# Optimization experiments

Measured on AMD Instinct MI355X. Metric: run time of the kernel, lower is better.

Reference implementation:

```python
import jax, jax.numpy as jnp
import numpy as np

B, S, T, H, E, V = 64, 512, 12, 256, 256, 50000


def _xavier(key, shape):
    lim = np.sqrt(6.0 / (shape[0] + shape[1]))
    return jax.random.uniform(key, shape, jnp.float32, -lim, lim)


def setup_inputs() -> dict:
    key = jax.random.key(0)
    ks = jax.random.split(key, 14)
    return {
        "input_ids": jax.random.randint(ks[0], (B, S), 0, V),
        "tree_ids": jax.random.randint(ks[1], (B, T, S), 0, S),
        "tree_ids_r": jax.random.randint(ks[2], (B, T, S), 0, S),
        "tree_ids_l": jax.random.randint(ks[3], (B, T, S), 0, S),
        "emb": _xavier(ks[4], (V, E)),
        "W_ioux": _xavier(ks[5], (E, 3 * H)),
        "b_ioux": jnp.zeros((3 * H,), jnp.float32),
        "U_iou_r": _xavier(ks[6], (H, 3 * H)),
        "U_iou_l": _xavier(ks[7], (H, 3 * H)),
        "W_f": _xavier(ks[8], (E, H)),
        "b_f": jnp.zeros((H,), jnp.float32),
        "U_f0": _xavier(ks[9], (H, H)),
        "U_f1": _xavier(ks[10], (H, H)),
        "U_f2": _xavier(ks[11], (H, H)),
        "U_f3": _xavier(ks[12], (H, H)),
    }


def reference(input_ids, tree_ids, tree_ids_r, tree_ids_l, emb,
              W_ioux, b_ioux, U_iou_r, U_iou_l, W_f, b_f,
              U_f0, U_f1, U_f2, U_f3):
    x = emb[input_ids]                      # [B, S, E]
    Bn, Sn = x.shape[0], x.shape[1]
    Hn = U_f0.shape[0]
    bidx = jnp.arange(Bn)[:, None]          # [B, 1] batch index for scatter

    def take(a, idx):                       # gather along node dim: out[b,s]=a[b,idx[b,s]]
        return jnp.take_along_axis(a, idx[..., None], axis=1)

    iou_x = x @ W_ioux + b_ioux             # precompute; constant across steps
    f_x = x @ W_f + b_f

    def step(carry, ids):
        h, c = carry
        td, tr, tl = ids                    # each [B, S]
        # which parent nodes receive children this step (node 0 excluded)
        counts = jnp.zeros((Bn, Sn), x.dtype).at[bidx, td].add(1.0)
        mask = (counts.at[:, 0].set(0.0) > 0)[..., None]  # [B, S, 1]
        # scatter-add child hidden projections into parent iou preactivations
        iou = iou_x.at[bidx, tr].add(h @ U_iou_r)
        iou = iou.at[bidx, tl].add(h @ U_iou_l)
        i, o, u = jnp.split(iou, 3, axis=-1)
        i, o, u = jax.nn.sigmoid(i), jax.nn.sigmoid(o), jnp.tanh(u)
        # forget gate per child: gather parent fx and child-hidden projections
        f = jax.nn.sigmoid(take(f_x, td)
                           + take(h @ U_f0 + h @ U_f1, tr)
                           + take(h @ U_f2 + h @ U_f3, tl))
        c_new = (i * u).at[bidx, td].add(f * c)
        h_new = o * jnp.tanh(c_new)
        h = jnp.where(mask, h_new, h)
        c = jnp.where(mask, c_new, c)
        return (h, c), None

    h0 = jnp.zeros((Bn, Sn, Hn), x.dtype)
    ids = (jnp.swapaxes(tree_ids, 0, 1),
           jnp.swapaxes(tree_ids_r, 0, 1),
           jnp.swapaxes(tree_ids_l, 0, 1))   # [T, B, S]
    (h, c), _ = jax.lax.scan(step, (h0, h0), ids)

    roots = tree_ids[:, -1, :].max(axis=1)   # [B]
    h_root = h[jnp.arange(Bn), roots]        # [B, H]
    return h, c, h_root
```

## Files before the change

### kernel.cpp

```cpp
#include <hip/hip_runtime.h>
#include <stdint.h>

#define B_ 64
#define S_ 512
#define T_ 12
#define M_ (B_*S_)
#define NP_ 2048

typedef __attribute__((ext_vector_type(8))) short bf16x8;
typedef __attribute__((ext_vector_type(4))) float f32x4;

__device__ __forceinline__ uint16_t f2bf(float f){
  union { float f; uint32_t u; } x; x.f = f;
  uint32_t r = x.u + 0x7FFFu + ((x.u >> 16) & 1u);
  return (uint16_t)(r >> 16);
}
__device__ __forceinline__ float bf2f(uint16_t u){
  union { float f; uint32_t u; } x; x.u = ((uint32_t)u) << 16; return x.f;
}
__device__ __forceinline__ float sigm(float x){ return 1.0f/(1.0f + expf(-x)); }
__device__ __forceinline__ float4 bf4(const uint16_t* p){
  const ushort4 v = *reinterpret_cast<const ushort4*>(p);
  return make_float4(bf2f(v.x), bf2f(v.y), bf2f(v.z), bf2f(v.w));
}

__device__ __forceinline__ void gload16(const uint16_t* g, uint16_t* l){
  __builtin_amdgcn_global_load_lds(
      (const __attribute__((address_space(1))) uint32_t*)g,
      (__attribute__((address_space(3))) uint32_t*)l, 16, 0, 0);
}

__global__ void zero16(uint4* __restrict__ p, long n16){
  const long i = (long)blockIdx.x * 256 + threadIdx.x;
  if (i < n16) p[i] = make_uint4(0,0,0,0);
}
__global__ void bf16_to_f32(const uint16_t* __restrict__ src, float* __restrict__ dst, long n){
  const long i = ((long)blockIdx.x * 256 + threadIdx.x) * 4;
  if (i + 3 < n) {
    const float4 o = bf4(src + i);
    *reinterpret_cast<float4*>(dst + i) = o;
  }
}

__global__ void build_ucatT(const float* __restrict__ Ur, const float* __restrict__ Ul,
                            const float* __restrict__ f0, const float* __restrict__ f1,
                            const float* __restrict__ f2, const float* __restrict__ f3,
                            uint16_t* __restrict__ UcatT){
  const int idx = blockIdx.x * 256 + threadIdx.x;
  const int n = idx >> 8, k = idx & 255;
  float v;
  if (n < 768)        v = Ur[k*768 + n];
  else if (n < 1536)  v = Ul[k*768 + (n-768)];
  else if (n < 1792) { int j = n-1536; v = f0[k*256+j] + f1[k*256+j]; }
  else               { int j = n-1792; v = f2[k*256+j] + f3[k*256+j]; }
  UcatT[(long)n*256 + k] = f2bf(v);
}

__global__ void build_wallT(const float* __restrict__ Wioux, const float* __restrict__ Wf,
                            uint16_t* __restrict__ WT){
  const int idx = blockIdx.x * 256 + threadIdx.x;
  const int n = idx >> 8, k = idx & 255;
  const float v = (n < 768) ? Wioux[(long)k*768 + n] : Wf[(long)k*256 + (n-768)];
  WT[(long)n*256 + k] = f2bf(v);
}

__global__ __launch_bounds__(256)
void mfma_gemm(const float* __restrict__ Af, const int* __restrict__ row_ids,
               const uint16_t* __restrict__ BT,
               const float* __restrict__ bias, const float* __restrict__ bias2, int split,
               uint16_t* __restrict__ C, int N)
{
  __shared__ uint16_t As[128][40];
  __shared__ uint16_t Bs[128][40];
  const int tid  = threadIdx.x;
  const int lane = tid & 63;
  const int wave = tid >> 6;
  const int wr = wave >> 1, wc = wave & 1;
  const long m0 = (long)blockIdx.y * 128;
  const int  n0 = blockIdx.x * 128;

  const int srow = tid >> 1;
  const int sseg = (tid & 1) * 16;
  const long arid = (long)row_ids[m0 + srow];

  f32x4 acc[4][4];
  #pragma unroll
  for (int i=0;i<4;i++)
    #pragma unroll
    for (int j=0;j<4;j++) acc[i][j] = (f32x4){0.f,0.f,0.f,0.f};

  for (int ks = 0; ks < 256; ks += 32) {
    {
      const float* sf = Af + arid*256 + ks + sseg;
      uint16_t tmp[16];
      #pragma unroll
      for (int e=0;e<16;e++) tmp[e] = f2bf(sf[e]);
      *reinterpret_cast<uint4*>(&As[srow][sseg])     = *reinterpret_cast<const uint4*>(&tmp[0]);
      *reinterpret_cast<uint4*>(&As[srow][sseg + 8]) = *reinterpret_cast<const uint4*>(&tmp[8]);
    }
    {
      const uint16_t* src = BT + (long)(n0 + srow)*256 + ks + sseg;
      *reinterpret_cast<uint4*>(&Bs[srow][sseg])     = *reinterpret_cast<const uint4*>(src);
      *reinterpret_cast<uint4*>(&Bs[srow][sseg + 8]) = *reinterpret_cast<const uint4*>(src + 8);
    }
    __syncthreads();

    bf16x8 af[4], bfv[4];
    #pragma unroll
    for (int i=0;i<4;i++)
      af[i] = *reinterpret_cast<const bf16x8*>(&As[wr*64 + i*16 + (lane & 15)][(lane >> 4)*8]);
    #pragma unroll
    for (int j=0;j<4;j++)
      bfv[j] = *reinterpret_cast<const bf16x8*>(&Bs[wc*64 + j*16 + (lane & 15)][(lane >> 4)*8]);
    #pragma unroll
    for (int i=0;i<4;i++)
      #pragma unroll
      for (int j=0;j<4;j++)
        acc[i][j] = __builtin_amdgcn_mfma_f32_16x16x32_bf16(af[i], bfv[j], acc[i][j], 0, 0, 0);
    __syncthreads();
  }

  const int col16 = lane & 15, rquad = lane >> 4;
  #pragma unroll
  for (int j=0;j<4;j++){
    const int col = n0 + wc*64 + j*16 + col16;
    const float bv = (col < split) ? bias[col] : bias2[col - split];
    #pragma unroll
    for (int i=0;i<4;i++){
      const long rbase = m0 + wr*64 + i*16 + rquad*4;
      #pragma unroll
      for (int r=0;r<4;r++)
        C[(rbase + r)*N + col] = f2bf(acc[i][j][r] + bv);
    }
  }
}

__global__ __launch_bounds__(256)
void gemm_step(const uint16_t* __restrict__ A, const uint16_t* __restrict__ BT,
               uint16_t* __restrict__ C, int N)
{
  __shared__ __align__(16) uint16_t As[2][4096];
  __shared__ __align__(16) uint16_t Bs[2][4096];
  const int tid = threadIdx.x, lane = tid & 63, wave = tid >> 6;
  const int wr = wave >> 1, wc = wave & 1;
  const long m0 = (long)blockIdx.y * 128;
  const int  n0 = blockIdx.x * 128;

  const int rl0 = wave*32 + (lane >> 2);
  const int rl1 = rl0 + 16;
  const int sg0 = (lane & 3) ^ ((rl0 >> 1) & 3);
  const int sg1 = (lane & 3) ^ ((rl1 >> 1) & 3);
  const uint16_t* ga0 = A + (m0 + rl0)*256 + sg0*8;
  const uint16_t* ga1 = A + (m0 + rl1)*256 + sg1*8;
  const uint16_t* gb0 = BT + (long)(n0 + rl0)*256 + sg0*8;
  const uint16_t* gb1 = BT + (long)(n0 + rl1)*256 + sg1*8;

  f32x4 acc[4][4];
  #pragma unroll
  for (int i=0;i<4;i++)
    #pragma unroll
    for (int j=0;j<4;j++) acc[i][j] = (f32x4){0.f,0.f,0.f,0.f};

  const int l15 = lane & 15, lseg = lane >> 4;
  int aoff[4], boff[4];
  #pragma unroll
  for (int i=0;i<4;i++){ const int m = wr*64 + i*16 + l15; aoff[i] = m*32 + ((lseg ^ ((m>>1)&3))<<3); }
  #pragma unroll
  for (int j=0;j<4;j++){ const int n = wc*64 + j*16 + l15; boff[j] = n*32 + ((lseg ^ ((n>>1)&3))<<3); }

  {
    uint16_t* a = &As[0][wave*1024];
    uint16_t* b = &Bs[0][wave*1024];
    gload16(ga0, a); gload16(ga1, a + 512);
    gload16(gb0, b); gload16(gb1, b + 512);
  }
  asm volatile("s_waitcnt vmcnt(0)" ::: "memory");
  __builtin_amdgcn_s_barrier();

  #pragma unroll
  for (int tt = 0; tt < 8; ++tt) {
    if (tt < 7) {
      const int nb = (tt + 1) & 1;
      const int ks = (tt + 1) * 32;
      uint16_t* a = &As[nb][wave*1024];
      uint16_t* b = &Bs[nb][wave*1024];
      gload16(ga0 + ks, a); gload16(ga1 + ks, a + 512);
      gload16(gb0 + ks, b); gload16(gb1 + ks, b + 512);
    }
    const int cb = tt & 1;
    bf16x8 af[4], bfv[4];
    #pragma unroll
    for (int i=0;i<4;i++) af[i]  = *reinterpret_cast<const bf16x8*>(&As[cb][aoff[i]]);
    #pragma unroll
    for (int j=0;j<4;j++) bfv[j] = *reinterpret_cast<const bf16x8*>(&Bs[cb][boff[j]]);
    #pragma unroll
    for (int i=0;i<4;i++)
      #pragma unroll
      for (int j=0;j<4;j++)
        acc[i][j] = __builtin_amdgcn_mfma_f32_16x16x32_bf16(af[i], bfv[j], acc[i][j], 0, 0, 0);
    if (tt < 7) {
      asm volatile("s_waitcnt vmcnt(0)" ::: "memory");
      __builtin_amdgcn_s_barrier();
    }
  }

  const int rquad = lane >> 4;
  #pragma unroll
  for (int j=0;j<4;j++){
    const int col = n0 + wc*64 + j*16 + l15;
    #pragma unroll
    for (int i=0;i<4;i++){
      const long rbase = m0 + wr*64 + i*16 + rquad*4;
      #pragma unroll
      for (int r=0;r<4;r++)
        C[(rbase + r)*N + col] = f2bf(acc[i][j][r]);
    }
  }
}

__global__ void build_csr(const int* __restrict__ td_g, const int* __restrict__ tr_g,
                          const int* __restrict__ tl_g,
                          int* __restrict__ csr_off, int* __restrict__ csr_val){
  const int t = blockIdx.x >> 6;
  const int b = blockIdx.x & 63;
  __shared__ int ids[S_];
  __shared__ int cnt[S_];
  __shared__ int off[S_];
  __shared__ int chc[8][S_];
  const int s = threadIdx.x;
  const int q = s >> 6;
  const int* srcs[3] = {td_g, tr_g, tl_g};
  for (int arr = 0; arr < 3; ++arr) {
    const int myid = srcs[arr][((long)b*T_ + t)*S_ + s];
    ids[s] = myid;
    cnt[s] = 0;
    #pragma unroll
    for (int qq=0; qq<8; qq++) chc[qq][s] = 0;
    __syncthreads();
    atomicAdd(&cnt[myid], 1);
    atomicAdd(&chc[q][myid], 1);
    __syncthreads();
    int rank = 0;
    for (int qq = 0; qq < q; ++qq) rank += chc[qq][myid];
    for (int i = q*64; i < s; ++i) rank += (ids[i] == myid) ? 1 : 0;
    off[s] = cnt[s];
    __syncthreads();
    for (int w = 1; w < S_; w <<= 1){
      const int v = (s >= w) ? off[s-w] : 0;
      __syncthreads();
      off[s] += v;
      __syncthreads();
    }
    const long base = (((long)arr*T_ + t)*B_ + b);
    int* offs = csr_off + base*(S_+1);
    int* vals = csr_val + base*S_;
    offs[s] = off[s] - cnt[s];
    if (s == S_-1) offs[S_] = off[s];
    vals[(off[myid] - cnt[myid]) + rank] = s;
    __syncthreads();
  }
}

__global__ __launch_bounds__(256)
void step_update(const uint16_t* __restrict__ h_in, const uint16_t* __restrict__ c_in,
                 uint16_t* __restrict__ h_out, uint16_t* __restrict__ c_out,
                 const uint16_t* __restrict__ P,
                 const uint16_t* __restrict__ ioufx,
                 const int* __restrict__ csr_off, const int* __restrict__ csr_val,
                 const int* __restrict__ tr_g, const int* __restrict__ tl_g,
                 int t, int row0)
{
  const int wave = threadIdx.x >> 6, lane = threadIdx.x & 63;
  const long bs = (long)row0 + (long)blockIdx.x*4 + wave;
  const int b = (int)(bs >> 9), s = (int)(bs & 511);
  const int j = lane * 4;

  const int* off_td = csr_off + (((long)0*T_ + t)*B_ + b)*(S_+1);
  const int td0 = off_td[s], td1 = off_td[s+1];
  const bool masked = (s != 0) && (td1 > td0);
  if (!masked) {
    *reinterpret_cast<ushort4*>(h_out + bs*256 + j) =
        *reinterpret_cast<const ushort4*>(h_in + bs*256 + j);
    *reinterpret_cast<ushort4*>(c_out + bs*256 + j) =
        *reinterpret_cast<const ushort4*>(c_in + bs*256 + j);
    return;
  }
  const int* off_tr = csr_off + (((long)1*T_ + t)*B_ + b)*(S_+1);
  const int* off_tl = csr_off + (((long)2*T_ + t)*B_ + b)*(S_+1);
  const int* val_td = csr_val + (((long)0*T_ + t)*B_ + b)*S_;
  const int* val_tr = csr_val + (((long)1*T_ + t)*B_ + b)*S_;
  const int* val_tl = csr_val + (((long)2*T_ + t)*B_ + b)*S_;

  const long lbase = (long)(b<<9) - row0;

  const long ib = bs*1024;
  float4 ai = bf4(ioufx + ib + j);
  float4 ao = bf4(ioufx + ib + 256 + j);
  float4 au = bf4(ioufx + ib + 512 + j);
  for (int p = off_tr[s]; p < off_tr[s+1]; ++p) {
    const long pr = (lbase + val_tr[p]) * NP_;
    const float4 x = bf4(P + pr + j), y = bf4(P + pr + 256 + j), z = bf4(P + pr + 512 + j);
    ai.x+=x.x; ai.y+=x.y; ai.z+=x.z; ai.w+=x.w;
    ao.x+=y.x; ao.y+=y.y; ao.z+=y.z; ao.w+=y.w;
    au.x+=z.x; au.y+=z.y; au.z+=z.z; au.w+=z.w;
  }
  for (int p = off_tl[s]; p < off_tl[s+1]; ++p) {
    const long pr = (lbase + val_tl[p]) * NP_;
    const float4 x = bf4(P + pr + 768 + j), y = bf4(P + pr + 1024 + j), z = bf4(P + pr + 1280 + j);
    ai.x+=x.x; ai.y+=x.y; ai.z+=x.z; ai.w+=x.w;
    ao.x+=y.x; ao.y+=y.y; ao.z+=y.z; ao.w+=y.w;
    au.x+=z.x; au.y+=z.y; au.z+=z.z; au.w+=z.w;
  }
  float4 cacc;
  cacc.x = sigm(ai.x)*tanhf(au.x); cacc.y = sigm(ai.y)*tanhf(au.y);
  cacc.z = sigm(ai.z)*tanhf(au.z); cacc.w = sigm(ai.w)*tanhf(au.w);
  const float4 fxv = bf4(ioufx + ib + 768 + j);
  const int* trrow = tr_g + ((long)b*T_ + t)*S_;
  const int* tlrow = tl_g + ((long)b*T_ + t)*S_;
  for (int p = td0; p < td1; ++p) {
    const int sp = val_td[p];
    const long prr = (lbase + trrow[sp]) * NP_ + 1536;
    const long prl = (lbase + tlrow[sp]) * NP_ + 1792;
    const float4 pa = bf4(P + prr + j), pb = bf4(P + prl + j);
    const float4 cv = bf4(c_in + ((long)(b<<9) + sp)*256 + j);
    cacc.x += sigm(fxv.x + pa.x + pb.x) * cv.x;
    cacc.y += sigm(fxv.y + pa.y + pb.y) * cv.y;
    cacc.z += sigm(fxv.z + pa.z + pb.z) * cv.z;
    cacc.w += sigm(fxv.w + pa.w + pb.w) * cv.w;
  }
  ushort4 ho, co;
  ho.x = f2bf(sigm(ao.x) * tanhf(cacc.x));
  ho.y = f2bf(sigm(ao.y) * tanhf(cacc.y));
  ho.z = f2bf(sigm(ao.z) * tanhf(cacc.z));
  ho.w = f2bf(sigm(ao.w) * tanhf(cacc.w));
  co.x = f2bf(cacc.x); co.y = f2bf(cacc.y); co.z = f2bf(cacc.z); co.w = f2bf(cacc.w);
  *reinterpret_cast<ushort4*>(h_out + bs*256 + j) = ho;
  *reinterpret_cast<ushort4*>(c_out + bs*256 + j) = co;
}

__global__ void root_kernel(const uint16_t* __restrict__ h, const int* __restrict__ td_g,
                            float* __restrict__ out_root){
  const int b = blockIdx.x;
  __shared__ int red[256];
  const int* td = td_g + ((long)b*T_ + (T_-1))*S_;
  int m = 0;
  for (int s = threadIdx.x; s < S_; s += 256) m = max(m, td[s]);
  red[threadIdx.x] = m; __syncthreads();
  for (int w = 128; w > 0; w >>= 1){
    if (threadIdx.x < w) red[threadIdx.x] = max(red[threadIdx.x], red[threadIdx.x+w]);
    __syncthreads();
  }
  const int root = red[0];
  out_root[b*256 + threadIdx.x] = bf2f(h[((long)b*512 + root)*256 + threadIdx.x]);
}

extern "C" void kernel_launch(void* const* d_in, const int* in_sizes, int n_in,
                              void* d_out, int out_size, void* d_ws, size_t ws_size,
                              hipStream_t stream) {
  const int*   input_ids  = (const int*)  d_in[0];
  const int*   tree_ids   = (const int*)  d_in[1];
  const int*   tree_ids_r = (const int*)  d_in[2];
  const int*   tree_ids_l = (const int*)  d_in[3];
  const float* emb        = (const float*)d_in[4];
  const float* W_ioux     = (const float*)d_in[5];
  const float* b_ioux     = (const float*)d_in[6];
  const float* W_f        = (const float*)d_in[9];
  const float* b_f        = (const float*)d_in[10];
  float* out = (float*)d_out;

  size_t woff = 0;
  auto alloc = [&](size_t bytes)->char*{
    char* p = (char*)d_ws + woff; woff += (bytes + 255) & ~(size_t)255; return p;
  };
  uint16_t* ioufx  = (uint16_t*)alloc((size_t)M_*1024*2);
  uint16_t* hA     = (uint16_t*)alloc((size_t)M_*256*2);
  uint16_t* cA     = (uint16_t*)alloc((size_t)M_*256*2);
  uint16_t* hB     = (uint16_t*)alloc((size_t)M_*256*2);
  uint16_t* cB     = (uint16_t*)alloc((size_t)M_*256*2);
  int* csr_off     = (int*)     alloc((size_t)3*T_*B_*(S_+1)*4);
  int* csr_val     = (int*)     alloc((size_t)3*T_*B_*S_*4);
  uint16_t* UcatT  = (uint16_t*)alloc((size_t)NP_*256*2);
  uint16_t* WallT  = (uint16_t*)alloc((size_t)1024*256*2);
  const int CB = 32;
  uint16_t* P      = (uint16_t*)alloc((size_t)CB*S_*NP_*2);

  build_ucatT<<<2048, 256, 0, stream>>>((const float*)d_in[7], (const float*)d_in[8],
      (const float*)d_in[11], (const float*)d_in[12], (const float*)d_in[13], (const float*)d_in[14],
      UcatT);
  build_wallT<<<1024, 256, 0, stream>>>(W_ioux, W_f, WallT);
  mfma_gemm<<<dim3(1024/128, M_/128), 256, 0, stream>>>(emb, input_ids, WallT,
                                                        b_ioux, b_f, 768, ioufx, 1024);
  build_csr<<<T_*B_, S_, 0, stream>>>(tree_ids, tree_ids_r, tree_ids_l, csr_off, csr_val);
  zero16<<<8192, 256, 0, stream>>>((uint4*)hA, 2097152L);

  uint16_t *hc = hA, *hn = hB, *cc = cA, *cn = cB;
  for (int t = 0; t < T_; ++t) {
    for (int b0 = 0; b0 < B_; b0 += CB) {
      const int row0 = b0 * S_;
      const int Mc   = CB * S_;
      gemm_step<<<dim3(NP_/128, Mc/128), 256, 0, stream>>>(
          hc + (long)row0*256, UcatT, P, NP_);
      step_update<<<Mc/4, 256, 0, stream>>>(hc, cc, hn, cn, P, ioufx,
                                            csr_off, csr_val, tree_ids_r, tree_ids_l,
                                            t, row0);
    }
    uint16_t* th = hc; hc = hn; hn = th;
    uint16_t* tc = cc; cc = cn; cn = tc;
  }

  bf16_to_f32<<<8192, 256, 0, stream>>>(hc, out, (long)M_*256);
  bf16_to_f32<<<8192, 256, 0, stream>>>(cc, out + (long)M_*256, (long)M_*256);
  root_kernel<<<B_, 256, 0, stream>>>(hc, tree_ids, out + 2L*M_*256);
}
```

Measured before the change: 1.375 ms.

## Update hidden state in place and remap GEMM/update blocks for XCD L2 locality

```diff
diff --git a/kernel.cpp b/kernel.cpp
--- a/kernel.cpp
+++ b/kernel.cpp
@@ -76,8 +76,11 @@
   const int lane = tid & 63;
   const int wave = tid >> 6;
   const int wr = wave >> 1, wc = wave & 1;
-  const long m0 = (long)blockIdx.y * 128;
-  const int  n0 = blockIdx.x * 128;
+  const int id = blockIdx.x, rx = id & 7, q = id >> 3;
+  const int mt = rx + 8*(q >> 3);
+  const int nt = q & 7;
+  const long m0 = (long)mt * 128;
+  const int  n0 = nt * 128;
 
   const int srow = tid >> 1;
   const int sseg = (tid & 1) * 16;
@@ -143,8 +146,11 @@
   __shared__ __align__(16) uint16_t Bs[2][4096];
   const int tid = threadIdx.x, lane = tid & 63, wave = tid >> 6;
   const int wr = wave >> 1, wc = wave & 1;
-  const long m0 = (long)blockIdx.y * 128;
-  const int  n0 = blockIdx.x * 128;
+  const int id = blockIdx.x, rx = id & 7, q = id >> 3;
+  const int mt = rx + 8*(q >> 4);
+  const int nt = q & 15;
+  const long m0 = (long)mt * 128;
+  const int  n0 = nt * 128;
 
   const int rl0 = wave*32 + (lane >> 2);
   const int rl1 = rl0 + 16;
@@ -262,8 +268,8 @@
 }
 
 __global__ __launch_bounds__(256)
-void step_update(const uint16_t* __restrict__ h_in, const uint16_t* __restrict__ c_in,
-                 uint16_t* __restrict__ h_out, uint16_t* __restrict__ c_out,
+void step_update(uint16_t* __restrict__ h,
+                 const uint16_t* __restrict__ c_in, uint16_t* __restrict__ c_out,
                  const uint16_t* __restrict__ P,
                  const uint16_t* __restrict__ ioufx,
                  const int* __restrict__ csr_off, const int* __restrict__ csr_val,
@@ -271,7 +277,10 @@
                  int t, int row0)
 {
   const int wave = threadIdx.x >> 6, lane = threadIdx.x & 63;
-  const long bs = (long)row0 + (long)blockIdx.x*4 + wave;
+  const int id = blockIdx.x, rx = id & 7, q = id >> 3;
+  const int b_local = rx + 8*(q >> 7);
+  const int rg = q & 127;
+  const long bs = (long)row0 + b_local*512 + rg*4 + wave;
   const int b = (int)(bs >> 9), s = (int)(bs & 511);
   const int j = lane * 4;
 
@@ -279,8 +288,6 @@
   const int td0 = off_td[s], td1 = off_td[s+1];
   const bool masked = (s != 0) && (td1 > td0);
   if (!masked) {
-    *reinterpret_cast<ushort4*>(h_out + bs*256 + j) =
-        *reinterpret_cast<const ushort4*>(h_in + bs*256 + j);
     *reinterpret_cast<ushort4*>(c_out + bs*256 + j) =
         *reinterpret_cast<const ushort4*>(c_in + bs*256 + j);
     return;
@@ -334,7 +341,7 @@
   ho.z = f2bf(sigm(ao.z) * tanhf(cacc.z));
   ho.w = f2bf(sigm(ao.w) * tanhf(cacc.w));
   co.x = f2bf(cacc.x); co.y = f2bf(cacc.y); co.z = f2bf(cacc.z); co.w = f2bf(cacc.w);
-  *reinterpret_cast<ushort4*>(h_out + bs*256 + j) = ho;
+  *reinterpret_cast<ushort4*>(h + bs*256 + j) = ho;
   *reinterpret_cast<ushort4*>(c_out + bs*256 + j) = co;
 }
 
@@ -375,7 +382,6 @@
   uint16_t* ioufx  = (uint16_t*)alloc((size_t)M_*1024*2);
   uint16_t* hA     = (uint16_t*)alloc((size_t)M_*256*2);
   uint16_t* cA     = (uint16_t*)alloc((size_t)M_*256*2);
-  uint16_t* hB     = (uint16_t*)alloc((size_t)M_*256*2);
   uint16_t* cB     = (uint16_t*)alloc((size_t)M_*256*2);
   int* csr_off     = (int*)     alloc((size_t)3*T_*B_*(S_+1)*4);
   int* csr_val     = (int*)     alloc((size_t)3*T_*B_*S_*4);
@@ -388,27 +394,23 @@
       (const float*)d_in[11], (const float*)d_in[12], (const float*)d_in[13], (const float*)d_in[14],
       UcatT);
   build_wallT<<<1024, 256, 0, stream>>>(W_ioux, W_f, WallT);
-  mfma_gemm<<<dim3(1024/128, M_/128), 256, 0, stream>>>(emb, input_ids, WallT,
-                                                        b_ioux, b_f, 768, ioufx, 1024);
+  mfma_gemm<<<2048, 256, 0, stream>>>(emb, input_ids, WallT, b_ioux, b_f, 768, ioufx, 1024);
   build_csr<<<T_*B_, S_, 0, stream>>>(tree_ids, tree_ids_r, tree_ids_l, csr_off, csr_val);
   zero16<<<8192, 256, 0, stream>>>((uint4*)hA, 2097152L);
 
-  uint16_t *hc = hA, *hn = hB, *cc = cA, *cn = cB;
+  uint16_t *cc = cA, *cn = cB;
   for (int t = 0; t < T_; ++t) {
     for (int b0 = 0; b0 < B_; b0 += CB) {
       const int row0 = b0 * S_;
-      const int Mc   = CB * S_;
-      gemm_step<<<dim3(NP_/128, Mc/128), 256, 0, stream>>>(
-          hc + (long)row0*256, UcatT, P, NP_);
-      step_update<<<Mc/4, 256, 0, stream>>>(hc, cc, hn, cn, P, ioufx,
+      gemm_step<<<2048, 256, 0, stream>>>(hA + (long)row0*256, UcatT, P, NP_);
+      step_update<<<4096, 256, 0, stream>>>(hA, cc, cn, P, ioufx,
                                             csr_off, csr_val, tree_ids_r, tree_ids_l,
                                             t, row0);
     }
-    uint16_t* th = hc; hc = hn; hn = th;
     uint16_t* tc = cc; cc = cn; cn = tc;
   }
 
-  bf16_to_f32<<<8192, 256, 0, stream>>>(hc, out, (long)M_*256);
+  bf16_to_f32<<<8192, 256, 0, stream>>>(hA, out, (long)M_*256);
   bf16_to_f32<<<8192, 256, 0, stream>>>(cc, out + (long)M_*256, (long)M_*256);
-  root_kernel<<<B_, 256, 0, stream>>>(hc, tree_ids, out + 2L*M_*256);
-}
+  root_kernel<<<B_, 256, 0, stream>>>(hA, tree_ids, out + 2L*M_*256);
+}
```

Result: faster. 1.321 ms (-3.9%).
